# Optimization experiments

Hardware: AMD Instinct MI355X
Metric: run time of the kernel (lower is better)

Reference implementation:

```python
import jax, jax.numpy as jnp
import numpy as np


def bilinear_sample(img, coords):
    # img: [N, H, W] correlation slices; coords: [N, K, K, 2] with (x, y) pixel coords.
    # Matches F.grid_sample(mode='bilinear', padding_mode='zeros', align_corners=True)
    # since the torch bilinear_sampler maps pixel coords to [-1,1] with align_corners=True.
    N, H, W = img.shape
    x = coords[..., 0]
    y = coords[..., 1]
    x0 = jnp.floor(x)
    y0 = jnp.floor(y)
    wx = x - x0  # weight toward x0+1
    wy = y - y0  # weight toward y0+1
    flat = img.reshape(N, H * W)

    def gather(yi, xi):
        valid = (xi >= 0) & (xi <= W - 1) & (yi >= 0) & (yi <= H - 1)
        xi_c = jnp.clip(xi, 0, W - 1).astype(jnp.int32)
        yi_c = jnp.clip(yi, 0, H - 1).astype(jnp.int32)
        idx = (yi_c * W + xi_c).reshape(N, -1)
        vals = jnp.take_along_axis(flat, idx, axis=1).reshape(xi.shape)
        return jnp.where(valid, vals, jnp.zeros((), img.dtype))

    v00 = gather(y0, x0)
    v01 = gather(y0, x0 + 1)
    v10 = gather(y0 + 1, x0)
    v11 = gather(y0 + 1, x0 + 1)
    return (v00 * (1 - wy) * (1 - wx) + v01 * (1 - wy) * wx
            + v10 * wy * (1 - wx) + v11 * wy * wx)


def corr_block(fmap1, fmap2, coords, num_levels, radius):
    B, D, H, W = fmap1.shape
    f1 = fmap1.reshape(B, D, H * W)
    f2 = fmap2.reshape(B, D, H * W)
    # [B, H1*W1, H2*W2] correlation volume, scaled by 1/sqrt(dim)
    corr = jnp.einsum('bdn,bdm->bnm', f1, f2) / jnp.sqrt(jnp.asarray(D, jnp.float32))
    corr = corr.reshape(B * H * W, H, W)

    pyramid = [corr]
    for _ in range(num_levels - 1):
        n, h, w = corr.shape
        # avg_pool2d(kernel=2, stride=2)
        corr = corr.reshape(n, h // 2, 2, w // 2, 2).mean(axis=(2, 4))
        pyramid.append(corr)

    r = radius
    d = jnp.linspace(-r, r, 2 * r + 1, dtype=jnp.float32)
    # meshgrid(dy, dx) stacked on last dim -> delta[...,0]=dy, delta[...,1]=dx
    delta = jnp.stack(jnp.meshgrid(d, d, indexing='ij'), axis=-1)  # [2r+1, 2r+1, 2]

    coords_q = coords.transpose(0, 2, 3, 1).reshape(B * H * W, 1, 1, 2)
    outs = []
    for i, c in enumerate(pyramid):
        coords_lvl = coords_q / (2 ** i) + delta[None]  # [N, 2r+1, 2r+1, 2]
        sampled = bilinear_sample(c, coords_lvl)        # [N, 2r+1, 2r+1]
        outs.append(sampled.reshape(B, H, W, -1))
    out = jnp.concatenate(outs, axis=-1)  # [B, H, W, num_levels*(2r+1)^2]
    return out.transpose(0, 3, 1, 2).astype(jnp.float32)


def setup_inputs() -> dict:
    key = jax.random.key(0)
    k1, k2, k3 = jax.random.split(key, 3)
    B, D, H, W = 4, 256, 64, 64
    fmap1 = jax.random.normal(k1, (B, D, H, W), dtype=jnp.float32)
    fmap2 = jax.random.normal(k2, (B, D, H, W), dtype=jnp.float32)
    coords = jax.random.uniform(k3, (B, 2, H, W), dtype=jnp.float32) * (W - 1)
    return {"fmap1": fmap1, "fmap2": fmap2, "coords": coords,
            "num_levels": 4, "radius": 4}


def reference(fmap1, fmap2, coords, num_levels, radius):
    return corr_block(fmap1, fmap2, coords, num_levels, radius)
```

## Files before the change

kernel.cpp:

```cpp
#include <hip/hip_runtime.h>

typedef unsigned short ushort_t;
typedef __attribute__((ext_vector_type(8))) short bfrag;
typedef __attribute__((ext_vector_type(4))) float f4;

#define NB 4
#define ND 256
#define NH 64
#define NW 64
#define NQ (NH * NW)
#define MPAD 5504
#define NLVL 4
#define NCH (NLVL * 81)

__device__ __forceinline__ float bf2f(ushort_t u) {
    return __uint_as_float(((unsigned)u) << 16);
}
__device__ __forceinline__ ushort_t f2bf(float f) {
    unsigned u = __float_as_uint(f);
    unsigned r = (u + 0x7fffu + ((u >> 16) & 1u)) >> 16;
    return (ushort_t)r;
}

__device__ __forceinline__ void gload_lds16(const void* g, void* l) {
    __builtin_amdgcn_global_load_lds(
        (const __attribute__((address_space(1))) unsigned int*)g,
        (__attribute__((address_space(3))) unsigned int*)l, 16, 0, 0);
}

__global__ __launch_bounds__(256) void sort_kernel(
    const float* __restrict__ coords,
    int* __restrict__ inv,
    int* __restrict__ tblS)
{
    __shared__ int hist[64];
    __shared__ int base[64];
    const int tid = threadIdx.x;
    const int b   = blockIdx.x;
    if (tid < 64) hist[tid] = 0;
    __syncthreads();
    int   keys[16];
    float cxs[16], cys[16];
#pragma unroll
    for (int i = 0; i < 16; i++) {
        int q = tid + i * 256;
        cxs[i] = coords[((size_t)b * 2 + 0) * NQ + q];
        cys[i] = coords[((size_t)b * 2 + 1) * NQ + q];
        keys[i] = (int)floorf(cys[i]);
        atomicAdd(&hist[keys[i]], 1);
    }
    __syncthreads();
    if (tid < 64) {
        int v = hist[tid];
        int s = v;
#pragma unroll
        for (int off = 1; off < 64; off <<= 1) {
            int o = __shfl_up(s, off);
            if (tid >= off) s += o;
        }
        base[tid] = s - v;
    }
    __syncthreads();
#pragma unroll
    for (int i = 0; i < 16; i++) {
        int q = tid + i * 256;
        int pos = atomicAdd(&base[keys[i]], 1);
        inv[(size_t)b * NQ + q] = pos;
#pragma unroll
        for (int lvl = 0; lvl < 4; lvl++) {
            float s = 1.0f / (float)(1 << lvl);
            int x0 = (int)floorf(cxs[i] * s);
            int y0 = (int)floorf(cys[i] * s);
            tblS[(((size_t)b * 4 + lvl) << 12) + pos] = x0 | (y0 << 6) | (q << 12);
        }
    }
}

__global__ __launch_bounds__(256) void pre_kernel(
    const float* __restrict__ f1, const float* __restrict__ f2,
    const int* __restrict__ inv,
    ushort_t* __restrict__ Abf, ushort_t* __restrict__ Ball)
{
    __shared__ float tile[64][65];
    const int tid = threadIdx.x;
    const int z = blockIdx.z;
    const int b = z & 3;
    const bool isA = (z < 4);
    const float* ib = (isA ? f1 : f2) + (size_t)b * ND * NQ;
    ushort_t* ob = isA ? (Abf + (size_t)b * NQ * ND) : (Ball + (size_t)b * MPAD * ND);
    const float scale = isA ? 0.0625f : 1.0f;
    const int n0 = blockIdx.x * 64, d0 = blockIdx.y * 64;
    const int nl = tid & 63, dg = tid >> 6;
#pragma unroll
    for (int i = 0; i < 16; i++) {
        int dl = dg + i * 4;
        tile[dl][nl] = ib[(size_t)(d0 + dl) * NQ + n0 + nl];
    }
    __syncthreads();
    const int dl = tid & 63, ng = tid >> 6;
    const int* invb = inv + (size_t)b * NQ;
#pragma unroll
    for (int i = 0; i < 16; i++) {
        int nn = ng + i * 4;
        int row = isA ? invb[n0 + nn] : (n0 + nn);
        ob[(size_t)row * ND + d0 + dl] = f2bf(tile[dl][nn] * scale);
    }
}

__global__ __launch_bounds__(256) void pool_fused(ushort_t* __restrict__ Ball)
{
    const int d = threadIdx.x;
    const int bid = blockIdx.x;
    const int b = bid >> 6;
    const int cell = bid & 63;
    const int Y = cell >> 3, X = cell & 7;
    ushort_t* base = Ball + (size_t)b * MPAD * ND;

    float s1[4][4];
#pragma unroll
    for (int iy = 0; iy < 4; iy++)
#pragma unroll
        for (int ix = 0; ix < 4; ix++) {
            int ry = 2 * (4 * Y + iy), rx = 2 * (4 * X + ix);
            float s = bf2f(base[(size_t)((ry    ) * 64 + rx    ) * ND + d])
                    + bf2f(base[(size_t)((ry    ) * 64 + rx + 1) * ND + d])
                    + bf2f(base[(size_t)((ry + 1) * 64 + rx    ) * ND + d])
                    + bf2f(base[(size_t)((ry + 1) * 64 + rx + 1) * ND + d]);
            s1[iy][ix] = s * 0.25f;
            base[(size_t)(4096 + (4 * Y + iy) * 32 + 4 * X + ix) * ND + d] = f2bf(s1[iy][ix]);
        }
    float s2[2][2];
#pragma unroll
    for (int iy = 0; iy < 2; iy++)
#pragma unroll
        for (int ix = 0; ix < 2; ix++) {
            float s = 0.25f * (s1[2*iy][2*ix] + s1[2*iy][2*ix+1]
                             + s1[2*iy+1][2*ix] + s1[2*iy+1][2*ix+1]);
            s2[iy][ix] = s;
            base[(size_t)(5120 + (2 * Y + iy) * 16 + 2 * X + ix) * ND + d] = f2bf(s);
        }
    float s3 = 0.25f * (s2[0][0] + s2[0][1] + s2[1][0] + s2[1][1]);
    base[(size_t)(5376 + Y * 8 + X) * ND + d] = f2bf(s3);
}

__global__ __launch_bounds__(512, 4) void gemm_corr(
    const ushort_t* __restrict__ A,
    const ushort_t* __restrict__ Bm,
    ushort_t* __restrict__ compact,
    const int* __restrict__ tblS)
{
    __shared__ ushort_t As[3][256 * 32];
    __shared__ ushort_t Bs[3][128 * 32];

    const int l   = blockIdx.x;
    const int wg  = (l & 7) * 344 + (l >> 3);
    const int z   = wg / 688;
    const int rem = wg - z * 688;
    const int by  = rem / 43;
    const int bxt = rem - by * 43;

    int lvl, mbase;
    if (bxt < 32)      { lvl = 0; mbase = bxt * 128; }
    else if (bxt < 40) { lvl = 1; mbase = 4096 + (bxt - 32) * 128; }
    else if (bxt < 42) { lvl = 2; mbase = 5120 + (bxt - 40) * 128; }
    else               { lvl = 3; mbase = 5376; }

    const int* tbL = tblS + (((size_t)z * 4 + lvl) << 12);

    if (lvl < 3) {
        int yF = (tbL[by * 256] >> 6) & 63;
        int yL = (tbL[by * 256 + 255] >> 6) & 63;
        int rlo, rhi;
        if (lvl == 0)      { rlo = bxt * 2;        rhi = rlo + 1; }
        else if (lvl == 1) { rlo = (bxt - 32) * 4; rhi = rlo + 3; }
        else               { rlo = (bxt - 40) * 8; rhi = rlo + 7; }
        if (rhi < yF - 4 || rlo > yL + 5) return;
    }

    const int tid  = threadIdx.x;
    const int lane = tid & 63;
    const int wv   = tid >> 6;
    const int wr   = wv >> 1;
    const int wc   = wv & 1;
    const int ln15 = lane & 15;
    const int g4   = lane >> 4;

    const ushort_t* Ab = A  + ((size_t)z * NQ   + (size_t)by * 256) * ND;
    const ushort_t* Bb = Bm + ((size_t)z * MPAD + (size_t)mbase) * ND;

    f4 acc[4][4] = {};

    const int rA  = tid >> 2;
    const int chA = (tid & 3) ^ ((tid >> 3) & 3);
    const ushort_t* srcA0 = Ab + (size_t)rA * ND + chA * 8;
    const ushort_t* srcA1 = srcA0 + (size_t)128 * ND;
    const ushort_t* srcB  = Bb + (size_t)rA * ND + chA * 8;

#define STAGE(buf, kk) {                                                   \
    gload_lds16(srcA0 + (kk), &As[buf][tid * 8]);                          \
    gload_lds16(srcA1 + (kk), &As[buf][(512 + tid) * 8]);                  \
    gload_lds16(srcB  + (kk), &Bs[buf][tid * 8]); }

    const int kch = (g4 ^ ((ln15 >> 1) & 3)) * 8;

    STAGE(0, 0);
    STAGE(1, 32);
    STAGE(2, 64);

#pragma unroll
    for (int t = 0; t < 8; ++t) {
        const int cur = t % 3;
        if (t < 6)       { asm volatile("s_waitcnt vmcnt(6)" ::: "memory"); }
        else if (t == 6) { asm volatile("s_waitcnt vmcnt(3)" ::: "memory"); }
        else             { asm volatile("s_waitcnt vmcnt(0)" ::: "memory"); }
        __builtin_amdgcn_s_barrier();
        asm volatile("" ::: "memory");

        bfrag a[4], bb[4];
#pragma unroll
        for (int mi = 0; mi < 4; mi++)
            a[mi] = *reinterpret_cast<const bfrag*>(
                &As[cur][(wr * 64 + mi * 16 + ln15) * 32 + kch]);
#pragma unroll
        for (int ni = 0; ni < 4; ni++)
            bb[ni] = *reinterpret_cast<const bfrag*>(
                &Bs[cur][(wc * 64 + ni * 16 + ln15) * 32 + kch]);

        if (t < 5) {
            __builtin_amdgcn_sched_barrier(0);
            asm volatile("s_waitcnt lgkmcnt(0)" ::: "memory");
            __builtin_amdgcn_s_barrier();
            asm volatile("" ::: "memory");
            STAGE(cur, (t + 3) * 32);
        }

#pragma unroll
        for (int mi = 0; mi < 4; mi++)
#pragma unroll
            for (int ni = 0; ni < 4; ni++)
                acc[mi][ni] = __builtin_amdgcn_mfma_f32_16x16x32_bf16(
                    a[mi], bb[ni], acc[mi][ni], 0, 0, 0);
    }
#undef STAGE

    const int row_base = by * 256 + wr * 64 + (g4 << 2);
    ushort_t* cmp      = compact + (size_t)z * NQ * 400 + lvl * 100;

    auto for_q = [&](auto body) {
#pragma unroll
        for (int mi = 0; mi < 4; mi++) {
            const int q0 = row_base + mi * 16;
            const int4 xy4 = *reinterpret_cast<const int4*>(&tbL[q0]);
            const int xys[4] = {xy4.x, xy4.y, xy4.z, xy4.w};
#pragma unroll
            for (int j = 0; j < 4; j++) {
                const int e = xys[j];
                body(mi, j, e & 63, (e >> 6) & 63, (size_t)((e >> 12) & 4095) * 400);
            }
        }
    };

    if (lvl == 0) {
        const int yfix = bxt * 2 + wc;
        for_q([&](int mi, int j, int x0, int y0, size_t qb) {
            unsigned v = (unsigned)(yfix - y0 + 4);
            if (v < 10u) {
                size_t vb = qb + v * 10;
#pragma unroll
                for (int ni = 0; ni < 4; ni++) {
                    unsigned u = (unsigned)(ln15 + 16 * ni + 4 - x0);
                    if (u < 10u) cmp[vb + u] = f2bf(acc[mi][ni][j]);
                }
            }
        });
    } else if (lvl == 1) {
        const int ybase = (bxt - 32) * 4 + wc * 2;
        for_q([&](int mi, int j, int x0, int y0, size_t qb) {
            unsigned u0 = (unsigned)(ln15 + 4 - x0), u1 = u0 + 16u;
            unsigned v0 = (unsigned)(ybase - y0 + 4), v1 = v0 + 1u;
            if (v0 < 10u) {
                if (u0 < 10u) cmp[qb + v0 * 10 + u0] = f2bf(acc[mi][0][j]);
                if (u1 < 10u) cmp[qb + v0 * 10 + u1] = f2bf(acc[mi][1][j]);
            }
            if (v1 < 10u) {
                if (u0 < 10u) cmp[qb + v1 * 10 + u0] = f2bf(acc[mi][2][j]);
                if (u1 < 10u) cmp[qb + v1 * 10 + u1] = f2bf(acc[mi][3][j]);
            }
        });
    } else if (lvl == 2) {
        const int ybase = (bxt - 40) * 8 + wc * 4;
        for_q([&](int mi, int j, int x0, int y0, size_t qb) {
            unsigned u = (unsigned)(ln15 + 4 - x0);
            if (u < 10u) {
#pragma unroll
                for (int ni = 0; ni < 4; ni++) {
                    unsigned v = (unsigned)(ybase + ni - y0 + 4);
                    if (v < 10u) cmp[qb + v * 10 + u] = f2bf(acc[mi][ni][j]);
                }
            }
        });
    } else if (wc == 0) {
        const int yb3 = ln15 >> 3;
        for_q([&](int mi, int j, int x0, int y0, size_t qb) {
            unsigned u = (unsigned)((ln15 & 7) + 4 - x0);
            if (u < 10u) {
#pragma unroll
                for (int ni = 0; ni < 4; ni++) {
                    unsigned v = (unsigned)(yb3 + 2 * ni - y0 + 4);
                    if (v < 10u) cmp[qb + v * 10 + u] = f2bf(acc[mi][ni][j]);
                }
            }
        });
    }
}

__global__ __launch_bounds__(256) void sample_kernel(
    const ushort_t* __restrict__ compact,
    const float* __restrict__ coords,
    float* __restrict__ out)
{
    __shared__ int   X0s[16], Y0s[16];
    __shared__ float wxs[16], wys[16];
    __shared__ float Dl[16 * 101];
    const int tid = threadIdx.x;
    const int g   = blockIdx.x;
    const int lvl = blockIdx.y;
    const int b   = blockIdx.z;
    const int Wl  = NW >> lvl;

    if (tid < 16) {
        int q = g * 16 + tid;
        float cx = coords[(size_t)(b * 2 + 0) * NQ + q];
        float cy = coords[(size_t)(b * 2 + 1) * NQ + q];
        float s = 1.0f / (float)(1 << lvl);
        float xl = cx * s, yl = cy * s;
        float fx = floorf(xl), fy = floorf(yl);
        X0s[tid] = (int)fx;
        Y0s[tid] = (int)fy;
        wxs[tid] = xl - fx;
        wys[tid] = yl - fy;
    }
    __syncthreads();

#pragma unroll
    for (int r = 0; r < 7; r++) {
        int e = r * 256 + tid;
        if (e < 16 * 100) {
            int qi = e / 100;
            int el = e - qi * 100;
            int v = el / 10;
            int u = el - v * 10;
            int xx = X0s[qi] - 4 + u;
            int yy = Y0s[qi] - 4 + v;
            float val = 0.f;
            if ((unsigned)xx < (unsigned)Wl && (unsigned)yy < (unsigned)Wl)
                val = bf2f(compact[((size_t)b * NQ + g * 16 + qi) * 400
                                   + lvl * 100 + el]);
            Dl[qi * 101 + el] = val;
        }
    }
    __syncthreads();

#pragma unroll
    for (int r = 0; r < 6; r++) {
        int e = r * 256 + tid;
        if (e < 16 * 81) {
            int qi = e & 15;
            int c = e >> 4;
            int i = c / 9;
            int j = c - i * 9;
            float wx = wxs[qi], wy = wys[qi];
            const float* dq = &Dl[qi * 101];
            float d00 = dq[j * 10 + i];
            float d10 = dq[j * 10 + i + 1];
            float d01 = dq[(j + 1) * 10 + i];
            float d11 = dq[(j + 1) * 10 + i + 1];
            float vx0 = d00 + wx * (d10 - d00);
            float vx1 = d01 + wx * (d11 - d01);
            float val = vx0 + wy * (vx1 - vx0);
            out[((size_t)b * NCH + lvl * 81 + c) * NQ + g * 16 + qi] = val;
        }
    }
}

extern "C" void kernel_launch(void* const* d_in, const int* in_sizes, int n_in,
                              void* d_out, int out_size, void* d_ws, size_t ws_size,
                              hipStream_t stream)
{
    const float* fmap1  = (const float*)d_in[0];
    const float* fmap2  = (const float*)d_in[1];
    const float* coords = (const float*)d_in[2];
    float* out = (float*)d_out;

    char* ws = (char*)d_ws;
    const size_t A_BYTES   = (size_t)NB * NQ * ND * 2;
    const size_t B_BYTES   = (size_t)NB * MPAD * ND * 2;
    const size_t CMP_BYTES = (size_t)NB * NQ * 400 * 2;
    const size_t TBL_BYTES = (size_t)NB * 4 * NQ * 4;
    ushort_t* Abf  = (ushort_t*)ws;
    ushort_t* Ball = (ushort_t*)(ws + A_BYTES);
    ushort_t* cmp  = (ushort_t*)(ws + A_BYTES + B_BYTES);
    int*      tblS = (int*)(ws + A_BYTES + B_BYTES + CMP_BYTES);
    int*      inv  = (int*)(ws + A_BYTES + B_BYTES + CMP_BYTES + TBL_BYTES);

    sort_kernel<<<NB, 256, 0, stream>>>(coords, inv, tblS);

    pre_kernel<<<dim3(64, 4, 8), 256, 0, stream>>>(fmap1, fmap2, inv, Abf, Ball);

    pool_fused<<<NB * 64, 256, 0, stream>>>(Ball);

    gemm_corr<<<dim3(16 * 43 * NB), 512, 0, stream>>>(Abf, Ball, cmp, tblS);

    sample_kernel<<<dim3(256, NLVL, NB), 256, 0, stream>>>(cmp, coords, out);
}
```

Before: 70.43 us.

## Gather sorted A rows in GEMM via perm; merge levels in sample kernel

The sort kernel now writes a forward permutation instead of an inverse one. pre_kernel stores A rows contiguously without scattering, and gemm_corr looks up each staged A row through the permutation, which turns the scattered stores into gathered loads. sample_kernel now handles all four pyramid levels in one block rather than one level per block, so each block reads a query's contiguous 400-element compact row once and launches four times fewer blocks. The cost is an extra indirection load in the GEMM prologue, rows that may be less contiguous, and more LDS per sample block.

```diff
diff --git a/kernel.cpp b/kernel.cpp
--- a/kernel.cpp
+++ b/kernel.cpp
@@ -30,7 +30,7 @@
 
 __global__ __launch_bounds__(256) void sort_kernel(
     const float* __restrict__ coords,
-    int* __restrict__ inv,
+    int* __restrict__ perm,
     int* __restrict__ tblS)
 {
     __shared__ int hist[64];
@@ -65,7 +65,7 @@
     for (int i = 0; i < 16; i++) {
         int q = tid + i * 256;
         int pos = atomicAdd(&base[keys[i]], 1);
-        inv[(size_t)b * NQ + q] = pos;
+        perm[(size_t)b * NQ + pos] = q;
 #pragma unroll
         for (int lvl = 0; lvl < 4; lvl++) {
             float s = 1.0f / (float)(1 << lvl);
@@ -78,7 +78,6 @@
 
 __global__ __launch_bounds__(256) void pre_kernel(
     const float* __restrict__ f1, const float* __restrict__ f2,
-    const int* __restrict__ inv,
     ushort_t* __restrict__ Abf, ushort_t* __restrict__ Ball)
 {
     __shared__ float tile[64][65];
@@ -98,12 +97,10 @@
     }
     __syncthreads();
     const int dl = tid & 63, ng = tid >> 6;
-    const int* invb = inv + (size_t)b * NQ;
 #pragma unroll
     for (int i = 0; i < 16; i++) {
         int nn = ng + i * 4;
-        int row = isA ? invb[n0 + nn] : (n0 + nn);
-        ob[(size_t)row * ND + d0 + dl] = f2bf(tile[dl][nn] * scale);
+        ob[(size_t)(n0 + nn) * ND + d0 + dl] = f2bf(tile[dl][nn] * scale);
     }
 }
 
@@ -147,6 +144,7 @@
     const ushort_t* __restrict__ A,
     const ushort_t* __restrict__ Bm,
     ushort_t* __restrict__ compact,
+    const int* __restrict__ perm,
     const int* __restrict__ tblS)
 {
     __shared__ ushort_t As[3][256 * 32];
@@ -185,15 +183,15 @@
     const int ln15 = lane & 15;
     const int g4   = lane >> 4;
 
-    const ushort_t* Ab = A  + ((size_t)z * NQ   + (size_t)by * 256) * ND;
     const ushort_t* Bb = Bm + ((size_t)z * MPAD + (size_t)mbase) * ND;
 
     f4 acc[4][4] = {};
 
     const int rA  = tid >> 2;
     const int chA = (tid & 3) ^ ((tid >> 3) & 3);
-    const ushort_t* srcA0 = Ab + (size_t)rA * ND + chA * 8;
-    const ushort_t* srcA1 = srcA0 + (size_t)128 * ND;
+    const int* pm = perm + (size_t)z * NQ + by * 256;
+    const ushort_t* srcA0 = A + ((size_t)z * NQ + pm[rA])       * ND + chA * 8;
+    const ushort_t* srcA1 = A + ((size_t)z * NQ + pm[128 + rA]) * ND + chA * 8;
     const ushort_t* srcB  = Bb + (size_t)rA * ND + chA * 8;
 
 #define STAGE(buf, kk) {                                                   \
@@ -319,66 +317,66 @@
     const float* __restrict__ coords,
     float* __restrict__ out)
 {
-    __shared__ int   X0s[16], Y0s[16];
-    __shared__ float wxs[16], wys[16];
-    __shared__ float Dl[16 * 101];
+    __shared__ float Dl[16][404];
+    __shared__ int   X0s[4][16], Y0s[4][16];
+    __shared__ float wxs[4][16], wys[4][16];
     const int tid = threadIdx.x;
     const int g   = blockIdx.x;
-    const int lvl = blockIdx.y;
-    const int b   = blockIdx.z;
-    const int Wl  = NW >> lvl;
-
-    if (tid < 16) {
-        int q = g * 16 + tid;
+    const int b   = blockIdx.y;
+
+    if (tid < 64) {
+        int qi = tid & 15, lvl = tid >> 4;
+        int q = g * 16 + qi;
         float cx = coords[(size_t)(b * 2 + 0) * NQ + q];
         float cy = coords[(size_t)(b * 2 + 1) * NQ + q];
         float s = 1.0f / (float)(1 << lvl);
         float xl = cx * s, yl = cy * s;
         float fx = floorf(xl), fy = floorf(yl);
-        X0s[tid] = (int)fx;
-        Y0s[tid] = (int)fy;
-        wxs[tid] = xl - fx;
-        wys[tid] = yl - fy;
-    }
-    __syncthreads();
-
-#pragma unroll
-    for (int r = 0; r < 7; r++) {
+        X0s[lvl][qi] = (int)fx;
+        Y0s[lvl][qi] = (int)fy;
+        wxs[lvl][qi] = xl - fx;
+        wys[lvl][qi] = yl - fy;
+    }
+    __syncthreads();
+
+#pragma unroll
+    for (int r = 0; r < 25; r++) {
         int e = r * 256 + tid;
-        if (e < 16 * 100) {
-            int qi = e / 100;
-            int el = e - qi * 100;
-            int v = el / 10;
-            int u = el - v * 10;
-            int xx = X0s[qi] - 4 + u;
-            int yy = Y0s[qi] - 4 + v;
-            float val = 0.f;
-            if ((unsigned)xx < (unsigned)Wl && (unsigned)yy < (unsigned)Wl)
-                val = bf2f(compact[((size_t)b * NQ + g * 16 + qi) * 400
-                                   + lvl * 100 + el]);
-            Dl[qi * 101 + el] = val;
-        }
-    }
-    __syncthreads();
-
-#pragma unroll
-    for (int r = 0; r < 6; r++) {
+        int qi = e / 400;
+        int el = e - qi * 400;
+        int lvl = el / 100;
+        int le = el - lvl * 100;
+        int v = le / 10, u = le - v * 10;
+        int xx = X0s[lvl][qi] - 4 + u;
+        int yy = Y0s[lvl][qi] - 4 + v;
+        int Wl = 64 >> lvl;
+        float val = 0.f;
+        if ((unsigned)xx < (unsigned)Wl && (unsigned)yy < (unsigned)Wl)
+            val = bf2f(compact[((size_t)b * NQ + g * 16 + qi) * 400 + el]);
+        Dl[qi][lvl * 101 + le] = val;
+    }
+    __syncthreads();
+
+#pragma unroll
+    for (int r = 0; r < 21; r++) {
         int e = r * 256 + tid;
-        if (e < 16 * 81) {
-            int qi = e & 15;
-            int c = e >> 4;
+        if (e < 5184) {
+            int lvl = e / 1296;
+            int rem = e - lvl * 1296;
+            int c  = rem >> 4;
+            int qi = rem & 15;
             int i = c / 9;
             int j = c - i * 9;
-            float wx = wxs[qi], wy = wys[qi];
-            const float* dq = &Dl[qi * 101];
+            float wx = wxs[lvl][qi], wy = wys[lvl][qi];
+            const float* dq = &Dl[qi][lvl * 101];
             float d00 = dq[j * 10 + i];
             float d10 = dq[j * 10 + i + 1];
             float d01 = dq[(j + 1) * 10 + i];
             float d11 = dq[(j + 1) * 10 + i + 1];
             float vx0 = d00 + wx * (d10 - d00);
             float vx1 = d01 + wx * (d11 - d01);
-            float val = vx0 + wy * (vx1 - vx0);
-            out[((size_t)b * NCH + lvl * 81 + c) * NQ + g * 16 + qi] = val;
+            out[((size_t)b * NCH + lvl * 81 + c) * NQ + g * 16 + qi]
+                = vx0 + wy * (vx1 - vx0);
         }
     }
 }
@@ -401,15 +399,15 @@
     ushort_t* Ball = (ushort_t*)(ws + A_BYTES);
     ushort_t* cmp  = (ushort_t*)(ws + A_BYTES + B_BYTES);
     int*      tblS = (int*)(ws + A_BYTES + B_BYTES + CMP_BYTES);
-    int*      inv  = (int*)(ws + A_BYTES + B_BYTES + CMP_BYTES + TBL_BYTES);
-
-    sort_kernel<<<NB, 256, 0, stream>>>(coords, inv, tblS);
-
-    pre_kernel<<<dim3(64, 4, 8), 256, 0, stream>>>(fmap1, fmap2, inv, Abf, Ball);
+    int*      perm = (int*)(ws + A_BYTES + B_BYTES + CMP_BYTES + TBL_BYTES);
+
+    sort_kernel<<<NB, 256, 0, stream>>>(coords, perm, tblS);
+
+    pre_kernel<<<dim3(64, 4, 8), 256, 0, stream>>>(fmap1, fmap2, Abf, Ball);
 
     pool_fused<<<NB * 64, 256, 0, stream>>>(Ball);
 
-    gemm_corr<<<dim3(16 * 43 * NB), 512, 0, stream>>>(Abf, Ball, cmp, tblS);
-
-    sample_kernel<<<dim3(256, NLVL, NB), 256, 0, stream>>>(cmp, coords, out);
-}
+    gemm_corr<<<dim3(16 * 43 * NB), 512, 0, stream>>>(Abf, Ball, cmp, perm, tblS);
+
+    sample_kernel<<<dim3(256, NB), 256, 0, stream>>>(cmp, coords, out);
+}
```

Result: slower. 76.62 us (+8.8%).
